# Optimization experiments

Measured on AMD Instinct MI355X. Metric: run time of the kernel, lower is better.

Reference implementation:

```python
import jax, jax.numpy as jnp
import numpy as np

EPS = 1e-6
CHUNK = 256
N_HEADS = 16
GATE_NORM = 16.0


def rmsnorm(x, eps=EPS):
    # RMSNorm without affine; normalizes over the last axis (matches custom
    # RMSNorm applied pre-view over full dim for q/k/v and over head_dim for subln)
    return x * jax.lax.rsqrt(jnp.mean(x * x, axis=-1, keepdims=True) + eps)


def chunk_gate_retention(q, k, v, gt, chunk_size):
    """Chunked gated linear attention (RetNet/GLA-style).
    Recurrence: S_t = exp(g_t) * S_{t-1} + k_t^T v_t;  o_t = q_t @ S_t.
    q,k,v: (b,h,t,d); gt: (b,h,t) log-decay. Returns (o, last_state)."""
    b, h, t, d = q.shape
    c = chunk_size
    n = t // c
    scale = d ** -0.5
    q = q.reshape(b, h, n, c, d) * scale
    k = k.reshape(b, h, n, c, d)
    v = v.reshape(b, h, n, c, d)
    g = gt.reshape(b, h, n, c)
    bc = jnp.cumsum(g, axis=-1)            # cumulative log-decay within chunk (incl. own gate)
    B = bc[..., -1:]                        # total chunk log-decay (b,h,n,1)
    # ---- intra-chunk (causal, decayed) ----
    decay = jnp.exp(bc[..., :, None] - bc[..., None, :])  # (b,h,n,c,c), <=1 on/below diag
    mask = jnp.tril(jnp.ones((c, c), dtype=bool))
    A = jnp.einsum('bhnid,bhnjd->bhnij', q, k) * jnp.where(mask, decay, 0.0)
    o_intra = jnp.einsum('bhnij,bhnjd->bhnid', A, v)
    # ---- per-chunk kv summaries (decay from position j to chunk end) ----
    kd = k * jnp.exp(B - bc)[..., None]
    kv = jnp.einsum('bhncd,bhnce->bhnde', kd, v)          # (b,h,n,d,d)
    qd = q * jnp.exp(bc)[..., None]                        # state decay into position i
    # ---- inter-chunk recurrence over chunk index ----
    def step(S, inp):
        qd_n, kv_n, B_n = inp
        o_cross = jnp.einsum('bhcd,bhde->bhce', qd_n, S)
        S_new = jnp.exp(B_n)[..., None] * S + kv_n
        return S_new, o_cross
    S0 = jnp.zeros((b, h, d, d), dtype=q.dtype)
    inps = (jnp.moveaxis(qd, 2, 0), jnp.moveaxis(kv, 2, 0), jnp.moveaxis(B, 2, 0))
    S_last, o_cross = jax.lax.scan(step, S0, inps)
    o_cross = jnp.moveaxis(o_cross, 0, 2)                  # (b,h,n,c,d)
    o = (o_intra + o_cross).reshape(b, h, t, d)
    return o, S_last


def setup_inputs() -> dict:
    key = jax.random.key(0)
    ks = jax.random.split(key, 7)
    dim, nh = 1024, N_HEADS
    s = 0.03  # keep activations sane
    return {
        'x':   jax.random.normal(ks[0], (2, 8192, dim), dtype=jnp.float32),
        'Wq':  jax.random.normal(ks[1], (dim, dim), dtype=jnp.float32) * s,
        'Wk':  jax.random.normal(ks[2], (dim, dim), dtype=jnp.float32) * s,
        'Wv':  jax.random.normal(ks[3], (dim, dim), dtype=jnp.float32) * s,
        'Wg':  jax.random.normal(ks[4], (dim, dim), dtype=jnp.float32) * s,
        'Wgt': jax.random.normal(ks[5], (dim, nh), dtype=jnp.float32) * s,
        'Wo':  jax.random.normal(ks[6], (dim, dim), dtype=jnp.float32) * s,
    }


def reference(x, Wq, Wk, Wv, Wg, Wgt, Wo):
    b, t, dim = x.shape
    h = N_HEADS
    d = dim // h
    q = rmsnorm(x @ Wq)
    k = rmsnorm(x @ Wk)
    v = rmsnorm(x @ Wv)
    g = x @ Wg
    gt = jax.nn.log_sigmoid(x @ Wgt) / GATE_NORM   # (b,t,h)
    qr = q.reshape(b, t, h, d).transpose(0, 2, 1, 3)
    kr = k.reshape(b, t, h, d).transpose(0, 2, 1, 3)
    vr = v.reshape(b, t, h, d).transpose(0, 2, 1, 3)
    gtr = gt.transpose(0, 2, 1)                    # (b,h,t)
    o, _ = chunk_gate_retention(qr, kr, vr, gtr, CHUNK)
    o = rmsnorm(o)                                 # subln over head_dim
    o = o.transpose(0, 2, 1, 3).reshape(b, t, dim)
    o = jax.nn.silu(g) * o                         # swiglu(g, o)
    return o @ Wo
```

## Files before the change

### kernel.cpp

```cpp
#include <hip/hip_runtime.h>

#define T_SEQ 8192
#define NH 16
#define HD 64
#define DIM 1024
#define ROWS 16384
#define CHK 256
#define NCHK 32

typedef float f32x4 __attribute__((ext_vector_type(4)));
typedef __bf16 bf16x8 __attribute__((ext_vector_type(8)));
typedef short short8 __attribute__((ext_vector_type(8)));
typedef short short4v __attribute__((ext_vector_type(4)));
typedef unsigned short ushort_t;

__device__ __forceinline__ float bf2f(ushort_t u){ return __uint_as_float(((unsigned)u)<<16); }
__device__ __forceinline__ ushort_t f2bf(float f){
  unsigned u = __float_as_uint(f);
  u += 0x7FFFu + ((u>>16)&1u);
  return (ushort_t)(u>>16);
}
#define BFLO(u) __uint_as_float((u)<<16)
#define BFHI(u) __uint_as_float((u)&0xFFFF0000u)
#define MFMA16(a,b,c) __builtin_amdgcn_mfma_f32_16x16x32_bf16((a),(b),(c),0,0,0)

__global__ __launch_bounds__(256) void transpose_all(const float* __restrict__ Wq,
    const float* __restrict__ Wk, const float* __restrict__ Wv,
    const float* __restrict__ Wg, const float* __restrict__ Wo,
    ushort_t* __restrict__ wcat, ushort_t* __restrict__ wot){
  int z = blockIdx.z;
  const float* W = (z==0)?Wq:(z==1)?Wk:(z==2)?Wv:(z==3)?Wg:Wo;
  ushort_t* D = (z<4)? (wcat + (size_t)z*DIM*DIM) : wot;
  __shared__ float tile[64][65];
  int k0 = blockIdx.x*64, n0 = blockIdx.y*64;
  int tid = threadIdx.x;
  #pragma unroll
  for (int it=0; it<16; ++it){
    int idx = tid + it*256;
    int r = idx>>6, c = idx&63;
    tile[r][c] = W[(size_t)(k0+r)*DIM + n0+c];
  }
  __syncthreads();
  #pragma unroll
  for (int it=0; it<16; ++it){
    int idx = tid + it*256;
    int r = idx>>6, c = idx&63;
    D[(size_t)(n0+r)*DIM + k0+c] = f2bf(tile[c][r]);
  }
}

__global__ __launch_bounds__(256,2) void cast_gt_ker(const float* __restrict__ x,
    const float* __restrict__ Wgt, ushort_t* __restrict__ xbf, float* __restrict__ gtb){
  __shared__ __align__(16) ushort_t As[64*64];
  __shared__ __align__(16) ushort_t wgt_t[16*1040];
  int tid = threadIdx.x, lane = tid&63, w = tid>>6;
  int r0 = blockIdx.x*64;
  #pragma unroll 4
  for (int i=0;i<64;++i){
    int idx = tid + i*256;
    wgt_t[(idx&15)*1040 + (idx>>4)] = f2bf(Wgt[idx]);
  }
  int arow = tid>>2;
  int acg = (tid&3)*2;
  const float* xrow = &x[(size_t)(r0+arow)*1024 + (tid&3)*16];
  ushort_t* xbrow = &xbf[(size_t)(r0+arow)*1024 + (tid&3)*16];
  int aslot0 = ((acg   ^ (arow&7))<<3);
  int aslot1 = (((acg+1) ^ (arow&7))<<3);
  f32x4 acc = {0.f,0.f,0.f,0.f};
  float4 f0 = *(const float4*)&xrow[0];
  float4 f1 = *(const float4*)&xrow[4];
  float4 f2 = *(const float4*)&xrow[8];
  float4 f3 = *(const float4*)&xrow[12];
  __syncthreads();
  for (int kt=0; kt<16; ++kt){
    ushort_t c[16] = { f2bf(f0.x),f2bf(f0.y),f2bf(f0.z),f2bf(f0.w),
                       f2bf(f1.x),f2bf(f1.y),f2bf(f1.z),f2bf(f1.w),
                       f2bf(f2.x),f2bf(f2.y),f2bf(f2.z),f2bf(f2.w),
                       f2bf(f3.x),f2bf(f3.y),f2bf(f3.z),f2bf(f3.w) };
    *(short8*)&xbrow[kt*64]   = *(short8*)&c[0];
    *(short8*)&xbrow[kt*64+8] = *(short8*)&c[8];
    *(short8*)&As[arow*64 + aslot0] = *(short8*)&c[0];
    *(short8*)&As[arow*64 + aslot1] = *(short8*)&c[8];
    if (kt < 15){
      f0 = *(const float4*)&xrow[(kt+1)*64 + 0];
      f1 = *(const float4*)&xrow[(kt+1)*64 + 4];
      f2 = *(const float4*)&xrow[(kt+1)*64 + 8];
      f3 = *(const float4*)&xrow[(kt+1)*64 +12];
    }
    __syncthreads();
    #pragma unroll
    for (int kk=0;kk<2;++kk){
      int row = w*16 + (lane&15);
      int g = kk*4 + (lane>>4);
      bf16x8 af = *(const bf16x8*)&As[row*64 + ((g^(row&7))<<3)];
      bf16x8 bfr = *(const bf16x8*)&wgt_t[(lane&15)*1040 + kt*64 + kk*32 + (lane>>4)*8];
      acc = MFMA16(af, bfr, acc);
    }
    __syncthreads();
  }
  #pragma unroll
  for (int r=0;r<4;++r){
    int grow = r0 + w*16 + (lane>>4)*4 + r;
    int bb = grow>>13, t = grow&(T_SEQ-1);
    float z = acc[r];
    float ls = fminf(z,0.f) - log1pf(__expf(-fabsf(z)));
    gtb[((size_t)(bb*NH + (lane&15)))*T_SEQ + t] = ls*(1.f/16.f);
  }
}

template<int OUT_BF16>
__global__ __launch_bounds__(256,2) void gemm_bt(const ushort_t* __restrict__ A,
    const ushort_t* __restrict__ Bt, void* __restrict__ Cv, int M, int N, int K,
    float* __restrict__ ssqp, int yoff){
  __shared__ __align__(16) ushort_t As[128*64];
  __shared__ __align__(16) ushort_t Bs[128*64];
  int tid = threadIdx.x;
  int lane = tid & 63, wid = tid >> 6;
  int wr = wid >> 1, wc = wid & 1;
  int m0 = blockIdx.x * 128, n0 = blockIdx.y * 128;
  f32x4 acc[4][4] = {};
  int srow = tid >> 3;
  int sg = tid & 7;
  const int nkt = K >> 6;
  for (int kt = 0; kt < nkt; ++kt){
    short8 ra[4], rb[4];
    #pragma unroll
    for (int s = 0; s < 4; ++s){
      int row = s*32 + srow;
      int gl = sg ^ (row & 7);
      ra[s] = *(const short8*)&A[(size_t)(m0 + row)*K + kt*64 + gl*8];
      rb[s] = *(const short8*)&Bt[(size_t)(n0 + row)*K + kt*64 + gl*8];
    }
    __syncthreads();
    #pragma unroll
    for (int s = 0; s < 4; ++s){
      int row = s*32 + srow;
      *(short8*)&As[row*64 + sg*8] = ra[s];
      *(short8*)&Bs[row*64 + sg*8] = rb[s];
    }
    __syncthreads();
    #pragma unroll
    for (int kk = 0; kk < 2; ++kk){
      bf16x8 af[4], bfv[4];
      #pragma unroll
      for (int m = 0; m < 4; ++m){
        int row = wr*64 + m*16 + (lane & 15);
        int g = kk*4 + (lane >> 4);
        af[m] = *(const bf16x8*)&As[row*64 + ((g ^ (row & 7))<<3)];
      }
      #pragma unroll
      for (int n = 0; n < 4; ++n){
        int row = wc*64 + n*16 + (lane & 15);
        int g = kk*4 + (lane >> 4);
        bfv[n] = *(const bf16x8*)&Bs[row*64 + ((g ^ (row & 7))<<3)];
      }
      #pragma unroll
      for (int m = 0; m < 4; ++m)
        #pragma unroll
        for (int n = 0; n < 4; ++n)
          acc[m][n] = MFMA16(af[m], bfv[n], acc[m][n]);
    }
  }
  #pragma unroll
  for (int m = 0; m < 4; ++m){
    int row = m0 + wr*64 + m*16 + (lane>>4)*4;
    #pragma unroll
    for (int n = 0; n < 4; ++n){
      int col = n0 + wc*64 + n*16 + (lane & 15);
      #pragma unroll
      for (int r = 0; r < 4; ++r){
        float v = acc[m][n][r];
        if (OUT_BF16) ((ushort_t*)Cv)[(size_t)(row+r)*N + col] = f2bf(v);
        else          ((float*)Cv)[(size_t)(row+r)*N + col] = v;
      }
    }
  }
  if (OUT_BF16 && (yoff + (int)blockIdx.y) < 24){
    int slot = (yoff + blockIdx.y)*2 + wc;
    #pragma unroll
    for (int m = 0; m < 4; ++m){
      #pragma unroll
      for (int r = 0; r < 4; ++r){
        float s = 0.f;
        #pragma unroll
        for (int n = 0; n < 4; ++n){ float xx = acc[m][n][r]; s += xx*xx; }
        s += __shfl_xor(s,1); s += __shfl_xor(s,2);
        s += __shfl_xor(s,4); s += __shfl_xor(s,8);
        if ((lane & 15) == 0){
          int row = m0 + wr*64 + m*16 + (lane>>4)*4 + r;
          ssqp[(size_t)slot*ROWS + row] = s;
        }
      }
    }
  }
}

__global__ __launch_bounds__(256) void rms_combine(const float* __restrict__ ssqp,
                                                   float* __restrict__ rmsb){
  int idx = blockIdx.x*256 + threadIdx.x;
  int mat = idx >> 14, row = idx & (ROWS-1);
  float s = 0.f;
  #pragma unroll
  for (int k=0;k<16;++k) s += ssqp[(size_t)(mat*16+k)*ROWS + row];
  rmsb[idx] = rsqrtf(s*(1.f/1024.f)+1e-6f);
}

__global__ __launch_bounds__(512,2) void attn_p1(const ushort_t* __restrict__ qkvg,
    const float* __restrict__ gtb, const float* __restrict__ rmsb,
    float* __restrict__ Bb, ushort_t* __restrict__ kvb){
  __shared__ __align__(16) ushort_t sh2[32768];
  __shared__ float bcf[256];
  __shared__ float tmp4[4];
  ushort_t* kdt = sh2;
  ushort_t* vt  = sh2 + 16384;
  int bid = blockIdx.x; int n = bid&31; int bh = bid>>5; int b = bh>>4; int h = bh&15;
  int t0 = n*CHK; int tid = threadIdx.x; int lane = tid&63; int w = tid>>6;
  float vscan = 0.f;
  if (tid < 256){
    vscan = gtb[(size_t)bh*T_SEQ + t0 + tid];
    #pragma unroll
    for (int off=1; off<64; off<<=1){ float u = __shfl_up(vscan, off); if (lane>=off) vscan += u; }
    if (lane==63) tmp4[w] = vscan;
  }
  __syncthreads();
  float Bn = tmp4[0]+tmp4[1]+tmp4[2]+tmp4[3];
  if (tid < 256){
    float pre=0;
    #pragma unroll
    for (int i=0;i<4;++i) if (i<w) pre += tmp4[i];
    bcf[tid] = vscan + pre;
  }
  if (tid==0) Bb[bid] = Bn;
  __syncthreads();
  {
    int j = tid>>1, dh = tid&1;
    int grow = b*T_SEQ + t0 + j;
    size_t rowb = (size_t)grow*4096;
    float fk = rmsb[ROWS + grow] * __expf(Bn - bcf[j]);
    float fv = rmsb[2*ROWS + grow];
    #pragma unroll
    for (int q8=0; q8<4; ++q8){
      short8 k8 = *(const short8*)&qkvg[rowb + 1024 + h*HD + dh*32 + q8*8];
      short8 v8 = *(const short8*)&qkvg[rowb + 2048 + h*HD + dh*32 + q8*8];
      #pragma unroll
      for (int kk=0; kk<8; ++kk){
        int d = dh*32 + q8*8 + kk;
        kdt[(d<<8) + (((j>>3)^(d&7))<<3) + (j&7)] = f2bf(bf2f((ushort_t)k8[kk])*fk);
        vt [(d<<8) + (((j>>3)^(d&7))<<3) + (j&7)] = f2bf(bf2f((ushort_t)v8[kk])*fv);
      }
    }
  }
  __syncthreads();
  if (w < 4){
    f32x4 acc[4] = {};
    #pragma unroll
    for (int s=0; s<8; ++s){
      int d = w*16 + (lane&15);
      int jj = s*32 + (lane>>4)*8;
      bf16x8 ka = *(const bf16x8*)&kdt[(d<<8) + (((jj>>3)^(d&7))<<3)];
      #pragma unroll
      for (int et=0; et<4; ++et){
        int e = et*16 + (lane&15);
        bf16x8 vf = *(const bf16x8*)&vt[(e<<8) + (((jj>>3)^(e&7))<<3)];
        acc[et] = MFMA16(ka, vf, acc[et]);
      }
    }
    ushort_t* kvp = &kvb[(size_t)bid*4096];
    #pragma unroll
    for (int et=0; et<4; ++et)
      #pragma unroll
      for (int r=0; r<4; ++r)
        kvp[(et*16 + (lane&15))*64 + w*16 + (lane>>4)*4 + r] = f2bf(acc[et][r]);
  }
}

__global__ __launch_bounds__(256) void scan_ker(const ushort_t* __restrict__ kvb,
    const float* __restrict__ Bb, ushort_t* __restrict__ Sb){
  int gidx = blockIdx.x*256 + threadIdx.x;
  int bh = gidx >> 12; int f = gidx & 4095;
  float S = 0.f;
  const ushort_t* kp = &kvb[(size_t)bh*NCHK*4096 + f];
  ushort_t* sp = &Sb[(size_t)bh*NCHK*4096 + f];
  for (int n=0;n<NCHK;++n){
    sp[(size_t)n*4096] = f2bf(S);
    S = __expf(Bb[bh*NCHK+n])*S + bf2f(kp[(size_t)n*4096]);
  }
}

__global__ __launch_bounds__(512,2) void attn_p3(const ushort_t* __restrict__ qkvg,
    const float* __restrict__ gtb, const float* __restrict__ rmsb,
    const ushort_t* __restrict__ Sb, ushort_t* __restrict__ oact){
  __shared__ __align__(16) ushort_t sh[(32768+16384+1024+32+2048)/2];
  ushort_t* vt = sh;
  ushort_t* ps = sh + 16384;
  float* bcs = (float*)(sh + 24576);
  float* tmp = (float*)(sh + 25088);
  float* rqs = (float*)(sh + 25104);
  float* rks = (float*)(sh + 25616);
  int bid = blockIdx.x; int n = bid&31; int bh = bid>>5; int b = bh>>4; int h = bh&15;
  int t0 = n*CHK; int tid = threadIdx.x; int lane = tid&63; int w = tid>>6;
  int wrow = w*32;
  size_t chunkbase = (size_t)b*T_SEQ + t0;
  int qcol = lane & 15, hi = lane >> 4;
  bf16x8 qf[2][2];
  #pragma unroll
  for (int rt=0; rt<2; ++rt)
    #pragma unroll
    for (int s=0; s<2; ++s)
      qf[rt][s] = *(const bf16x8*)&qkvg[(chunkbase + wrow + rt*16 + qcol)*4096
                                        + h*HD + s*32 + hi*8];
  float vscan = 0.f;
  if (tid < 256){
    vscan = gtb[(size_t)bh*T_SEQ + t0 + tid];
    #pragma unroll
    for (int off=1; off<64; off<<=1){ float u = __shfl_up(vscan, off); if (lane>=off) vscan += u; }
    if (lane==63) tmp[w] = vscan;
  }
  __syncthreads();
  if (tid < 256){
    float pre=0;
    #pragma unroll
    for (int i=0;i<4;++i) if (i<w) pre += tmp[i];
    bcs[tid] = vscan + pre;
    int grow = b*T_SEQ + t0 + tid;
    rqs[tid] = rmsb[grow];
    rks[tid] = rmsb[ROWS + grow];
  }
  {
    int j = tid>>1, ehalf = tid&1;
    int grow = b*T_SEQ + t0 + j;
    size_t rowb = (size_t)grow*4096;
    float fv = rmsb[2*ROWS + grow];
    #pragma unroll
    for (int q8=0; q8<4; ++q8){
      short8 v8 = *(const short8*)&qkvg[rowb + 2048 + h*HD + ehalf*32 + q8*8];
      #pragma unroll
      for (int kk=0; kk<8; ++kk){
        int e = ehalf*32 + q8*8 + kk;
        vt[(e<<8) + (((j>>3)^(e&7))<<3) + (j&7)] = f2bf(bf2f((ushort_t)v8[kk])*fv);
      }
    }
  }
  __syncthreads();
  f32x4 o_[2][4] = {};
  #pragma unroll
  for (int s=0; s<2; ++s)
    #pragma unroll
    for (int et=0; et<4; ++et){
      bf16x8 stf = *(const bf16x8*)&Sb[(size_t)bid*4096 + (et*16 + qcol)*64 + s*32 + hi*8];
      #pragma unroll
      for (int rt=0; rt<2; ++rt)
        o_[rt][et] = MFMA16(qf[rt][s], stf, o_[rt][et]);
    }
  #pragma unroll
  for (int rt=0; rt<2; ++rt)
    #pragma unroll
    for (int rr=0; rr<4; ++rr){
      int ri = wrow + rt*16 + hi*4 + rr;
      float fs = 0.125f*__expf(bcs[ri])*rqs[ri];
      #pragma unroll
      for (int et=0; et<4; ++et) o_[rt][et][rr] *= fs;
    }
  float rqv[2], bqv[2];
  #pragma unroll
  for (int rt=0; rt<2; ++rt){
    int qr = wrow + rt*16 + qcol;
    rqv[rt] = rqs[qr]; bqv[rt] = bcs[qr];
  }
  int s0 = qcol + 32*(hi&1), s1 = s0 + 16;
  bool ctp = (hi >> 1) != 0;
  for (int hb=0; hb<=w; ++hb){
    int jbase = hb*32;
    bool dia = (hb == w);
    bf16x8 kf[2][2];
    #pragma unroll
    for (int s=0; s<2; ++s)
      #pragma unroll
      for (int ct=0; ct<2; ++ct)
        kf[s][ct] = *(const bf16x8*)&qkvg[(chunkbase + jbase + ct*16 + qcol)*4096
                                          + 1024 + h*HD + s*32 + hi*8];
    f32x4 s2[2][2] = {};
    #pragma unroll
    for (int s=0; s<2; ++s)
      #pragma unroll
      for (int ct=0; ct<2; ++ct)
        #pragma unroll
        for (int rt=0; rt<2; ++rt)
          s2[rt][ct] = MFMA16(kf[s][ct], qf[rt][s], s2[rt][ct]);
    bf16x8 vf[4];
    #pragma unroll
    for (int et=0; et<4; ++et){
      int e = et*16 + qcol;
      int jj = jbase + hi*8;
      vf[et] = *(const bf16x8*)&vt[(e<<8) + (((jj>>3) ^ (e&7))<<3)];
    }
    #pragma unroll
    for (int rt=0; rt<2; ++rt){
      int qr = wrow + rt*16 + qcol;
      unsigned wd[2][2];
      #pragma unroll
      for (int ct=0; ct<2; ++ct){
        float pv[4];
        #pragma unroll
        for (int rr=0; rr<4; ++rr){
          int kr = jbase + ct*16 + hi*4 + rr;
          float val = s2[rt][ct][rr] * 0.125f * rqv[rt] * rks[kr] * __expf(bqv[rt] - bcs[kr]);
          if (dia && kr > qr) val = 0.f;
          pv[rr] = val;
        }
        wd[ct][0] = ((unsigned)f2bf(pv[1])<<16) | f2bf(pv[0]);
        wd[ct][1] = ((unsigned)f2bf(pv[3])<<16) | f2bf(pv[2]);
      }
      unsigned a00 = (unsigned)__shfl((int)wd[0][0], s0);
      unsigned a10 = (unsigned)__shfl((int)wd[1][0], s0);
      unsigned a01 = (unsigned)__shfl((int)wd[0][1], s0);
      unsigned a11 = (unsigned)__shfl((int)wd[1][1], s0);
      unsigned b00 = (unsigned)__shfl((int)wd[0][0], s1);
      unsigned b10 = (unsigned)__shfl((int)wd[1][0], s1);
      unsigned b01 = (unsigned)__shfl((int)wd[0][1], s1);
      unsigned b11 = (unsigned)__shfl((int)wd[1][1], s1);
      union { unsigned u[4]; bf16x8 v; } pa;
      pa.u[0] = ctp ? a10 : a00;
      pa.u[1] = ctp ? a11 : a01;
      pa.u[2] = ctp ? b10 : b00;
      pa.u[3] = ctp ? b11 : b01;
      #pragma unroll
      for (int et=0; et<4; ++et)
        o_[rt][et] = MFMA16(pa.v, vf[et], o_[rt][et]);
    }
  }
  float rms8[2][4];
  #pragma unroll
  for (int rt=0; rt<2; ++rt)
    #pragma unroll
    for (int rr=0; rr<4; ++rr){
      float ssq = 0.f;
      #pragma unroll
      for (int et=0; et<4; ++et){ float xx = o_[rt][et][rr]; ssq += xx*xx; }
      ssq += __shfl_xor(ssq,1); ssq += __shfl_xor(ssq,2);
      ssq += __shfl_xor(ssq,4); ssq += __shfl_xor(ssq,8);
      rms8[rt][rr] = rsqrtf(ssq*(1.f/64.f)+1e-6f);
    }
  #pragma unroll
  for (int eh=0; eh<2; ++eh){
    #pragma unroll
    for (int rt=0; rt<2; ++rt)
      #pragma unroll
      for (int e2=0; e2<2; ++e2){
        int et = eh*2 + e2;
        #pragma unroll
        for (int rr=0; rr<4; ++rr){
          int pi = rt*16 + hi*4 + rr;
          int pj = e2*16 + qcol;
          ps[w*1024 + pi*32 + (((pj>>3) ^ ((pi>>2)&3))<<3) + (pj&7)] =
            f2bf(o_[rt][et][rr]*rms8[rt][rr]);
        }
      }
    int i2 = lane&31, e16 = (lane>>5)*16;
    int gr0 = e16>>3;
    int f = (i2>>2)&3;
    short8 ov0 = *(const short8*)&ps[w*1024 + i2*32 + ((gr0^f)<<3)];
    short8 ov1 = *(const short8*)&ps[w*1024 + i2*32 + (((gr0+1)^f)<<3)];
    size_t rowg = chunkbase + wrow + i2;
    short8 gv0 = *(const short8*)&qkvg[rowg*4096 + 3072 + h*HD + eh*32 + e16];
    short8 gv1 = *(const short8*)&qkvg[rowg*4096 + 3072 + h*HD + eh*32 + e16 + 8];
    ushort_t outv[16];
    #pragma unroll
    for (int k=0;k<8;++k){
      float gf = bf2f((ushort_t)gv0[k]);
      float sg = gf/(1.f+__expf(-gf));
      outv[k] = f2bf(bf2f((ushort_t)ov0[k])*sg);
    }
    #pragma unroll
    for (int k=0;k<8;++k){
      float gf = bf2f((ushort_t)gv1[k]);
      float sg = gf/(1.f+__expf(-gf));
      outv[8+k] = f2bf(bf2f((ushort_t)ov1[k])*sg);
    }
    ushort_t* op = &oact[rowg*DIM + h*HD + eh*32 + e16];
    *(short8*)&op[0] = *(short8*)&outv[0];
    *(short8*)&op[8] = *(short8*)&outv[8];
  }
}

extern "C" void kernel_launch(void* const* d_in, const int* in_sizes, int n_in,
                              void* d_out, int out_size, void* d_ws, size_t ws_size,
                              hipStream_t stream){
  const float* x  = (const float*)d_in[0];
  const float* Wq = (const float*)d_in[1];
  const float* Wk = (const float*)d_in[2];
  const float* Wv = (const float*)d_in[3];
  const float* Wg = (const float*)d_in[4];
  const float* Wgt= (const float*)d_in[5];
  const float* Wo = (const float*)d_in[6];
  float* out = (float*)d_out;

  char* p = (char*)d_ws;
  ushort_t* xbf  = (ushort_t*)p; p += (size_t)ROWS*DIM*2;
  ushort_t* wcat = (ushort_t*)p; p += (size_t)4*DIM*DIM*2;
  ushort_t* wot  = (ushort_t*)p; p += (size_t)DIM*DIM*2;
  ushort_t* qkvg = (ushort_t*)p; p += (size_t)ROWS*4096*2;
  float* gtb = (float*)p; p += (size_t)32*T_SEQ*4;
  float* Bb  = (float*)p; p += 1024*4;
  ushort_t* kvb = (ushort_t*)p; p += (size_t)1024*4096*2;
  ushort_t* Sb = (ushort_t*)p; p += (size_t)1024*4096*2;
  ushort_t* oact = (ushort_t*)p; p += (size_t)ROWS*DIM*2;
  float* ssqp = (float*)p; p += (size_t)48*ROWS*4;
  float* rmsb = (float*)p; p += (size_t)3*ROWS*4;
  if ((size_t)(p - (char*)d_ws) > ws_size) return;

  cast_gt_ker<<<ROWS/64,256,0,stream>>>(x, Wgt, xbf, gtb);
  transpose_all<<<dim3(16,16,5),256,0,stream>>>(Wq, Wk, Wv, Wg, Wo, wcat, wot);
  gemm_bt<1><<<dim3(ROWS/128, 4096/128), 256, 0, stream>>>(xbf, wcat, qkvg, ROWS, 4096, DIM, ssqp, 0);
  rms_combine<<<(3*ROWS)/256,256,0,stream>>>(ssqp, rmsb);
  attn_p1<<<1024,512,0,stream>>>(qkvg, gtb, rmsb, Bb, kvb);
  scan_ker<<<512,256,0,stream>>>(kvb, Bb, Sb);
  attn_p3<<<1024,512,0,stream>>>(qkvg, gtb, rmsb, Sb, oact);
  gemm_bt<0><<<dim3(ROWS/128, 1024/128), 256, 0, stream>>>(oact, wot, out, ROWS, 1024, DIM, nullptr, 0);
}
```

Before: 320.7 us.

## Switch GEMM to 32x32x16 MFMA and prefetch next K-tile into registers

```diff
diff --git a/kernel.cpp b/kernel.cpp
--- a/kernel.cpp
+++ b/kernel.cpp
@@ -9,6 +9,7 @@
 #define NCHK 32
 
 typedef float f32x4 __attribute__((ext_vector_type(4)));
+typedef float f32x16 __attribute__((ext_vector_type(16)));
 typedef __bf16 bf16x8 __attribute__((ext_vector_type(8)));
 typedef short short8 __attribute__((ext_vector_type(8)));
 typedef short short4v __attribute__((ext_vector_type(4)));
@@ -23,6 +24,7 @@
 #define BFLO(u) __uint_as_float((u)<<16)
 #define BFHI(u) __uint_as_float((u)&0xFFFF0000u)
 #define MFMA16(a,b,c) __builtin_amdgcn_mfma_f32_16x16x32_bf16((a),(b),(c),0,0,0)
+#define MFMA32(a,b,c) __builtin_amdgcn_mfma_f32_32x32x16_bf16((a),(b),(c),0,0,0)
 
 __global__ __launch_bounds__(256) void transpose_all(const float* __restrict__ Wq,
     const float* __restrict__ Wk, const float* __restrict__ Wv,
@@ -118,19 +120,20 @@
   int lane = tid & 63, wid = tid >> 6;
   int wr = wid >> 1, wc = wid & 1;
   int m0 = blockIdx.x * 128, n0 = blockIdx.y * 128;
-  f32x4 acc[4][4] = {};
+  f32x16 acc[2][2] = {};
   int srow = tid >> 3;
   int sg = tid & 7;
+  int l31 = lane & 31, hi = lane >> 5;
   const int nkt = K >> 6;
+  short8 ra[4], rb[4];
+  #pragma unroll
+  for (int s = 0; s < 4; ++s){
+    int row = s*32 + srow;
+    int gl = sg ^ (row & 7);
+    ra[s] = *(const short8*)&A[(size_t)(m0 + row)*K + gl*8];
+    rb[s] = *(const short8*)&Bt[(size_t)(n0 + row)*K + gl*8];
+  }
   for (int kt = 0; kt < nkt; ++kt){
-    short8 ra[4], rb[4];
-    #pragma unroll
-    for (int s = 0; s < 4; ++s){
-      int row = s*32 + srow;
-      int gl = sg ^ (row & 7);
-      ra[s] = *(const short8*)&A[(size_t)(m0 + row)*K + kt*64 + gl*8];
-      rb[s] = *(const short8*)&Bt[(size_t)(n0 + row)*K + kt*64 + gl*8];
-    }
     __syncthreads();
     #pragma unroll
     for (int s = 0; s < 4; ++s){
@@ -139,59 +142,64 @@
       *(short8*)&Bs[row*64 + sg*8] = rb[s];
     }
     __syncthreads();
-    #pragma unroll
-    for (int kk = 0; kk < 2; ++kk){
-      bf16x8 af[4], bfv[4];
-      #pragma unroll
-      for (int m = 0; m < 4; ++m){
-        int row = wr*64 + m*16 + (lane & 15);
-        int g = kk*4 + (lane >> 4);
-        af[m] = *(const bf16x8*)&As[row*64 + ((g ^ (row & 7))<<3)];
-      }
-      #pragma unroll
-      for (int n = 0; n < 4; ++n){
-        int row = wc*64 + n*16 + (lane & 15);
-        int g = kk*4 + (lane >> 4);
-        bfv[n] = *(const bf16x8*)&Bs[row*64 + ((g ^ (row & 7))<<3)];
-      }
-      #pragma unroll
-      for (int m = 0; m < 4; ++m)
+    if (kt+1 < nkt){
+      #pragma unroll
+      for (int s = 0; s < 4; ++s){
+        int row = s*32 + srow;
+        int gl = sg ^ (row & 7);
+        ra[s] = *(const short8*)&A[(size_t)(m0 + row)*K + (kt+1)*64 + gl*8];
+        rb[s] = *(const short8*)&Bt[(size_t)(n0 + row)*K + (kt+1)*64 + gl*8];
+      }
+    }
+    #pragma unroll
+    for (int kk = 0; kk < 4; ++kk){
+      int g = kk*2 + hi;
+      bf16x8 af[2], bfv[2];
+      #pragma unroll
+      for (int tm = 0; tm < 2; ++tm){
+        int row = wr*64 + tm*32 + l31;
+        af[tm] = *(const bf16x8*)&As[row*64 + ((g ^ (row & 7))<<3)];
+      }
+      #pragma unroll
+      for (int tn = 0; tn < 2; ++tn){
+        int row = wc*64 + tn*32 + l31;
+        bfv[tn] = *(const bf16x8*)&Bs[row*64 + ((g ^ (row & 7))<<3)];
+      }
+      #pragma unroll
+      for (int tm = 0; tm < 2; ++tm)
         #pragma unroll
-        for (int n = 0; n < 4; ++n)
-          acc[m][n] = MFMA16(af[m], bfv[n], acc[m][n]);
-    }
-  }
-  #pragma unroll
-  for (int m = 0; m < 4; ++m){
-    int row = m0 + wr*64 + m*16 + (lane>>4)*4;
-    #pragma unroll
-    for (int n = 0; n < 4; ++n){
-      int col = n0 + wc*64 + n*16 + (lane & 15);
-      #pragma unroll
-      for (int r = 0; r < 4; ++r){
-        float v = acc[m][n][r];
-        if (OUT_BF16) ((ushort_t*)Cv)[(size_t)(row+r)*N + col] = f2bf(v);
-        else          ((float*)Cv)[(size_t)(row+r)*N + col] = v;
-      }
-    }
-  }
+        for (int tn = 0; tn < 2; ++tn)
+          acc[tm][tn] = MFMA32(af[tm], bfv[tn], acc[tm][tn]);
+    }
+  }
+  #pragma unroll
+  for (int tm = 0; tm < 2; ++tm)
+    #pragma unroll
+    for (int tn = 0; tn < 2; ++tn)
+      #pragma unroll
+      for (int r = 0; r < 16; ++r){
+        int row = m0 + wr*64 + tm*32 + (r&3) + 8*(r>>2) + 4*hi;
+        int col = n0 + wc*64 + tn*32 + l31;
+        float v = acc[tm][tn][r];
+        if (OUT_BF16) ((ushort_t*)Cv)[(size_t)row*N + col] = f2bf(v);
+        else          ((float*)Cv)[(size_t)row*N + col] = v;
+      }
   if (OUT_BF16 && (yoff + (int)blockIdx.y) < 24){
     int slot = (yoff + blockIdx.y)*2 + wc;
     #pragma unroll
-    for (int m = 0; m < 4; ++m){
-      #pragma unroll
-      for (int r = 0; r < 4; ++r){
+    for (int tm = 0; tm < 2; ++tm)
+      #pragma unroll
+      for (int r = 0; r < 16; ++r){
         float s = 0.f;
         #pragma unroll
-        for (int n = 0; n < 4; ++n){ float xx = acc[m][n][r]; s += xx*xx; }
-        s += __shfl_xor(s,1); s += __shfl_xor(s,2);
-        s += __shfl_xor(s,4); s += __shfl_xor(s,8);
-        if ((lane & 15) == 0){
-          int row = m0 + wr*64 + m*16 + (lane>>4)*4 + r;
+        for (int tn = 0; tn < 2; ++tn){ float xx = acc[tm][tn][r]; s += xx*xx; }
+        s += __shfl_xor(s,1); s += __shfl_xor(s,2); s += __shfl_xor(s,4);
+        s += __shfl_xor(s,8); s += __shfl_xor(s,16);
+        if (l31 == 0){
+          int row = m0 + wr*64 + tm*32 + (r&3) + 8*(r>>2) + 4*hi;
           ssqp[(size_t)slot*ROWS + row] = s;
         }
       }
-    }
   }
 }
 
```

Result: slower. 355.6 us (+10.9%).
